# Performance work log

Measured on AMD Instinct MI355X. Metric: run time of the kernel, lower is better.

Reference implementation:

```python
import jax, jax.numpy as jnp
import numpy as np

D_MODEL = 768
N_HEADS_CFG = 12
D_STATE = 32
D_CONV = 4
EXPAND = 2
HEADDIM = D_MODEL // N_HEADS_CFG          # 64
D_INNER = EXPAND * D_MODEL                # 1536
NHEADS = D_INNER // HEADDIM               # 24 (Mamba2 internal heads)
CONV_DIM = D_INNER + 2 * D_STATE          # 1600
D_IN_PROJ = 2 * D_INNER + 2 * D_STATE + NHEADS  # 3160
EPS = 1e-5
B_SZ, SEQ = 2, 512


def rmsnorm(x, w):
    return x * jax.lax.rsqrt(jnp.mean(x * x, axis=-1, keepdims=True) + EPS) * w


def mamba2(u, Wi, cw, cb, dtb, Alog, Dp, nw, Wo):
    """Mamba2 mixer: in_proj -> causal depthwise conv(silu) -> selective scan -> gated RMSNorm -> out_proj."""
    b, l, _ = u.shape
    zxbcdt = u @ Wi.T                                   # [b,l,d_in_proj]
    z, xBC, dt = jnp.split(zxbcdt, [D_INNER, D_INNER + CONV_DIM], axis=-1)
    # causal depthwise conv over time
    xBC = jnp.transpose(xBC, (0, 2, 1))                 # [b,c,l]
    xBC = jax.lax.conv_general_dilated(
        xBC, cw[:, None, :], window_strides=(1,),
        padding=[(D_CONV - 1, 0)], feature_group_count=CONV_DIM)
    xBC = jax.nn.silu(jnp.transpose(xBC + cb[None, :, None], (0, 2, 1)))
    x, Bm, Cm = jnp.split(xBC, [D_INNER, D_INNER + D_STATE], axis=-1)
    x = x.reshape(b, l, NHEADS, HEADDIM)                # [b,l,h,p]
    dt = jax.nn.softplus(dt + dtb)                      # [b,l,h]
    A = -jnp.exp(Alog)                                  # [h]
    a = jnp.exp(dt * A)                                 # decay [b,l,h]
    # dt * x outer B  -> [b,l,h,p,n]
    dBx = (dt[..., None, None] * x[..., None]) * Bm[:, :, None, None, :]

    def combine(e1, e2):
        a1, h1 = e1
        a2, h2 = e2
        return (a1 * a2, a2[..., None, None] * h1 + h2)

    _, h = jax.lax.associative_scan(combine, (a, dBx), axis=1)  # h: [b,l,h,p,n]
    y = jnp.einsum('blhpn,bln->blhp', h, Cm) + Dp[None, None, :, None] * x
    y = y.reshape(b, l, D_INNER)
    y = rmsnorm(y * jax.nn.silu(z), nw)                 # gated RMSNorm
    return y @ Wo.T                                     # [b,l,d_model]


def _mamba_params(key, scale=0.02):
    ks = jax.random.split(key, 6)
    return dict(
        in_w=jax.random.normal(ks[0], (D_IN_PROJ, D_MODEL), jnp.float32) * scale,
        conv_w=jax.random.normal(ks[1], (CONV_DIM, D_CONV), jnp.float32) * scale,
        conv_b=jnp.zeros((CONV_DIM,), jnp.float32),
        dt_bias=jax.random.uniform(ks[2], (NHEADS,), jnp.float32, -4.0, -1.0),
        A_log=jnp.log(jax.random.uniform(ks[3], (NHEADS,), jnp.float32, 1.0, 16.0)),
        D=jnp.ones((NHEADS,), jnp.float32),
        norm_w=jnp.ones((D_INNER,), jnp.float32),
        out_w=jax.random.normal(ks[4], (D_MODEL, D_INNER), jnp.float32) * scale,
    )


def setup_inputs() -> dict:
    key = jax.random.key(0)
    kx, kf, kb, ko = jax.random.split(key, 4)
    f = _mamba_params(kf)
    bw = _mamba_params(kb)
    return {
        'x': jax.random.normal(kx, (B_SZ, SEQ, D_MODEL), jnp.float32),
        'norm_w': jnp.ones((D_MODEL,), jnp.float32),
        'fwd_in_w': f['in_w'], 'fwd_conv_w': f['conv_w'], 'fwd_conv_b': f['conv_b'],
        'fwd_dt_bias': f['dt_bias'], 'fwd_A_log': f['A_log'], 'fwd_D': f['D'],
        'fwd_norm_w': f['norm_w'], 'fwd_out_w': f['out_w'],
        'bwd_in_w': bw['in_w'], 'bwd_conv_w': bw['conv_w'], 'bwd_conv_b': bw['conv_b'],
        'bwd_dt_bias': bw['dt_bias'], 'bwd_A_log': bw['A_log'], 'bwd_D': bw['D'],
        'bwd_norm_w': bw['norm_w'], 'bwd_out_w': bw['out_w'],
        'out_proj_w': jax.random.normal(ko, (D_MODEL, 2 * D_MODEL), jnp.float32) * 0.02,
    }


def reference(x, norm_w,
              fwd_in_w, fwd_conv_w, fwd_conv_b, fwd_dt_bias, fwd_A_log, fwd_D, fwd_norm_w, fwd_out_w,
              bwd_in_w, bwd_conv_w, bwd_conv_b, bwd_dt_bias, bwd_A_log, bwd_D, bwd_norm_w, bwd_out_w,
              out_proj_w):
    h = rmsnorm(x, norm_w)
    f_out = mamba2(h, fwd_in_w, fwd_conv_w, fwd_conv_b, fwd_dt_bias, fwd_A_log, fwd_D, fwd_norm_w, fwd_out_w)
    b_out = mamba2(h[:, ::-1], bwd_in_w, bwd_conv_w, bwd_conv_b, bwd_dt_bias, bwd_A_log, bwd_D, bwd_norm_w, bwd_out_w)[:, ::-1]
    return x + jnp.concatenate([f_out, b_out], axis=-1) @ out_proj_w.T
```

## Files before the change

kernel.cpp:

```cpp
#include <hip/hip_runtime.h>
#include <hip/hip_bf16.h>

#define DMODEL 768
#define DINNER 1536
#define DSTATE 32
#define NHEADS 24
#define HEADDIM 64
#define CONVDIM 1600
#define DINPROJ 3160
#define NPAD 3200
#define SEQ 512
#define MROWS 1024
#define CL 64
#define NCH 8

typedef __attribute__((ext_vector_type(8))) short bf16x8;
typedef __attribute__((ext_vector_type(4))) float f32x4;

__device__ __forceinline__ ushort f2bs(float v) {
  __hip_bfloat16 b = __float2bfloat16(v);
  return __builtin_bit_cast(unsigned short, b);
}

__device__ __forceinline__ void gld16(const void* g, const void* l) {
  __builtin_amdgcn_global_load_lds((const __attribute__((address_space(1))) void*)g,
                                   (__attribute__((address_space(3))) void*)l, 16, 0, 0);
}

__device__ __forceinline__ float block_reduce_sum(float v, float* ws4) {
#pragma unroll
  for (int o = 32; o > 0; o >>= 1) v += __shfl_xor(v, o, 64);
  int wid = threadIdx.x >> 6;
  if ((threadIdx.x & 63) == 0) ws4[wid] = v;
  __syncthreads();
  return ws4[0] + ws4[1] + ws4[2] + ws4[3];
}

__global__ __launch_bounds__(256) void f2b_all(
    const float* __restrict__ s0, const float* __restrict__ s1,
    const float* __restrict__ s2, const float* __restrict__ s3,
    const float* __restrict__ s4, ushort* __restrict__ d) {
  constexpr size_t NP_IN = (size_t)NPAD * DMODEL;
  constexpr size_t NE_IN = (size_t)DINPROJ * DMODEL;
  constexpr size_t NE_O = (size_t)DMODEL * DINNER;
  size_t i = ((size_t)blockIdx.x * 256 + threadIdx.x) * 4;
  const float* src;
  size_t off, ne;
  if (i < NP_IN) { src = s0; off = i; ne = NE_IN; }
  else if (i < 2 * NP_IN) { src = s1; off = i - NP_IN; ne = NE_IN; }
  else if (i < 2 * NP_IN + NE_O) { src = s2; off = i - 2 * NP_IN; ne = NE_O; }
  else if (i < 2 * NP_IN + 2 * NE_O) { src = s3; off = i - 2 * NP_IN - NE_O; ne = NE_O; }
  else if (i < 2 * NP_IN + 3 * NE_O) { src = s4; off = i - 2 * NP_IN - 2 * NE_O; ne = NE_O; }
  else return;
  ushort* dp = d + i;
  if (off + 3 < ne) {
    float4 v = *(const float4*)(src + off);
    dp[0] = f2bs(v.x); dp[1] = f2bs(v.y); dp[2] = f2bs(v.z); dp[3] = f2bs(v.w);
  } else {
#pragma unroll
    for (int j = 0; j < 4; ++j) dp[j] = (off + j < ne) ? f2bs(src[off + j]) : (ushort)0;
  }
}

__global__ __launch_bounds__(256) void rmsnorm_in_kernel(
    const float* __restrict__ x, const float* __restrict__ w, ushort* __restrict__ h) {
  __shared__ float ws4[4];
  int m = blockIdx.x;
  const float* xr = x + (size_t)m * DMODEL;
  float v[3];
  float ss = 0.f;
#pragma unroll
  for (int i = 0; i < 3; ++i) {
    v[i] = xr[threadIdx.x + i * 256];
    ss += v[i] * v[i];
  }
  ss = block_reduce_sum(ss, ws4);
  float sc = rsqrtf(ss / (float)DMODEL + 1e-5f);
  ushort* hr = h + (size_t)m * DMODEL;
#pragma unroll
  for (int i = 0; i < 3; ++i) {
    int c = threadIdx.x + i * 256;
    hr[c] = f2bs(v[i] * sc * w[c]);
  }
}

template <int BM, int BN, bool ADD_X, bool OUT_BF16>
__global__ __launch_bounds__(256) void gemm2(
    const ushort* __restrict__ A, int lda, size_t aZ,
    const ushort* __restrict__ Bw, int ldb, size_t bZ,
    void* __restrict__ Cout, int ldc, size_t cZ,
    const float* __restrict__ X, int ldx, int K) {
  constexpr int AG = BM / 16;
  constexpr int BG = BN / 16;
  constexpr int MR = BM / 32;
  constexpr int NR = BN / 32;
  __shared__ ushort As[2][BM * 32];
  __shared__ ushort Bs[2][BN * 32];
  const int t = threadIdx.x, w = t >> 6, l = t & 63;
  const int m0 = blockIdx.y * BM, n0 = blockIdx.x * BN;
  const int wr = w >> 1, wc = w & 1;
  const int fr = l & 15, fq = l >> 4;
  const int sr = l >> 2, sc2 = (l & 3) * 8;
  const ushort* Ap = A + (size_t)blockIdx.z * aZ;
  const ushort* Bp = Bw + (size_t)blockIdx.z * bZ;

  auto stage = [&](int bb, int k0) {
#pragma unroll
    for (int g = w; g < AG + BG; g += 4) {
      if (g < AG) {
        int row = g * 16 + sr;
        gld16(Ap + (size_t)(m0 + row) * lda + k0 + sc2, (const char*)&As[bb][0] + g * 1024);
      } else {
        int gg = g - AG;
        int row = gg * 16 + sr;
        gld16(Bp + (size_t)(n0 + row) * ldb + k0 + sc2, (const char*)&Bs[bb][0] + gg * 1024);
      }
    }
  };

  f32x4 acc[MR][NR];
#pragma unroll
  for (int m = 0; m < MR; ++m)
#pragma unroll
    for (int n = 0; n < NR; ++n) acc[m][n] = (f32x4){0.f, 0.f, 0.f, 0.f};

  stage(0, 0);
  __syncthreads();
  int cur = 0;
  const int nk = K / 32;
  for (int k = 0; k < nk; ++k) {
    if (k + 1 < nk) stage(cur ^ 1, (k + 1) * 32);
    bf16x8 af[MR], bfr[NR];
#pragma unroll
    for (int m = 0; m < MR; ++m)
      af[m] = *(const bf16x8*)&As[cur][(wr * (BM / 2) + m * 16 + fr) * 32 + fq * 8];
#pragma unroll
    for (int n = 0; n < NR; ++n)
      bfr[n] = *(const bf16x8*)&Bs[cur][(wc * (BN / 2) + n * 16 + fr) * 32 + fq * 8];
#pragma unroll
    for (int m = 0; m < MR; ++m)
#pragma unroll
      for (int n = 0; n < NR; ++n)
        acc[m][n] = __builtin_amdgcn_mfma_f32_16x16x32_bf16(af[m], bfr[n], acc[m][n], 0, 0, 0);
    __syncthreads();
    cur ^= 1;
  }

#pragma unroll
  for (int m = 0; m < MR; ++m) {
#pragma unroll
    for (int n = 0; n < NR; ++n) {
      int col = n0 + wc * (BN / 2) + n * 16 + fr;
#pragma unroll
      for (int j = 0; j < 4; ++j) {
        int row = m0 + wr * (BM / 2) + m * 16 + fq * 4 + j;
        float v = acc[m][n][j];
        if (ADD_X) v += X[(size_t)row * ldx + col];
        if (OUT_BF16)
          ((ushort*)Cout + (size_t)blockIdx.z * cZ)[(size_t)row * ldc + col] = f2bs(v);
        else
          ((float*)Cout + (size_t)blockIdx.z * cZ)[(size_t)row * ldc + col] = v;
      }
    }
  }
}

__global__ __launch_bounds__(256) void conv_dt_kernel(
    const float* __restrict__ zx,
    const float* __restrict__ cw0, const float* __restrict__ cb0,
    const float* __restrict__ dtb0, const float* __restrict__ Al0,
    const float* __restrict__ cw1, const float* __restrict__ cb1,
    const float* __restrict__ dtb1, const float* __restrict__ Al1,
    float* __restrict__ xbc, float* __restrict__ dta) {
  int m = blockIdx.x;
  int dir = blockIdx.y;
  int l = m & (SEQ - 1);
  const float* cw = dir ? cw1 : cw0;
  const float* cb = dir ? cb1 : cb0;
  const float* zrow = zx + (size_t)m * 6400 + dir * 3200 + DINNER;
  float* xo = xbc + ((size_t)dir * MROWS + m) * CONVDIM;
  for (int c = threadIdx.x; c < CONVDIM; c += 256) {
    float acc = cb[c];
    if (dir == 0) {
#pragma unroll
      for (int d = 0; d < 4; ++d) {
        if (l - d >= 0) acc = fmaf(zrow[-(size_t)d * 6400 + c], cw[c * 4 + 3 - d], acc);
      }
    } else {
#pragma unroll
      for (int d = 0; d < 4; ++d) {
        if (l + d < SEQ) acc = fmaf(zrow[(size_t)d * 6400 + c], cw[c * 4 + 3 - d], acc);
      }
    }
    xo[c] = acc / (1.f + expf(-acc));
  }
  if (threadIdx.x < NHEADS) {
    int hh = threadIdx.x;
    const float* dtb = dir ? dtb1 : dtb0;
    const float* Al = dir ? Al1 : Al0;
    float v = zx[(size_t)m * 6400 + dir * 3200 + DINNER + CONVDIM + hh] + dtb[hh];
    float dt = (v > 20.f) ? v : log1pf(expf(v));
    float A = -expf(Al[hh]);
    dta[((size_t)dir * MROWS + m) * 48 + hh] = dt;
    dta[((size_t)dir * MROWS + m) * 48 + NHEADS + hh] = expf(dt * A);
  }
}

__global__ __launch_bounds__(256) void scan_phase1(
    const float* __restrict__ xbc, const float* __restrict__ dta,
    float* __restrict__ sbuf, float* __restrict__ abuf) {
  __shared__ float xs[CL][64];
  __shared__ float bcs[CL][64];
  __shared__ float das[CL][2];
  int c = blockIdx.x, bh = blockIdx.y, dir = blockIdx.z;
  int b = bh / NHEADS, h = bh % NHEADS;
  int t = threadIdx.x, p = t >> 2, q = t & 3;
  const float* xb = xbc + ((size_t)dir * MROWS + b * SEQ) * CONVDIM;
  int lrow = t >> 4, lcol = (t & 15) * 4;
#pragma unroll
  for (int r = 0; r < 4; ++r) {
    int s = r * 16 + lrow;
    int tau = c * CL + s;
    int prow = dir ? (SEQ - 1 - tau) : tau;
    const float* rowp = xb + (size_t)prow * CONVDIM;
    *(float4*)&xs[s][lcol] = *(const float4*)(rowp + h * HEADDIM + lcol);
    *(float4*)&bcs[s][lcol] = *(const float4*)(rowp + DINNER + lcol);
  }
  if (t < 128) {
    int s = t >> 1, wsel = t & 1;
    int tau = c * CL + s;
    int prow = dir ? (SEQ - 1 - tau) : tau;
    das[s][wsel] = dta[((size_t)dir * MROWS + b * SEQ + prow) * 48 + wsel * NHEADS + h];
  }
  __syncthreads();
  float hst[8];
#pragma unroll
  for (int j = 0; j < 8; ++j) hst[j] = 0.f;
  float alpha = 1.f;
#pragma unroll 8
  for (int s = 0; s < CL; ++s) {
    float xp = xs[s][p];
    float dt_s = das[s][0], a_s = das[s][1];
    float cx = dt_s * xp;
    alpha *= a_s;
    float4 B0 = *(const float4*)&bcs[s][q * 8];
    float4 B1 = *(const float4*)&bcs[s][q * 8 + 4];
    float Bv[8] = {B0.x, B0.y, B0.z, B0.w, B1.x, B1.y, B1.z, B1.w};
#pragma unroll
    for (int j = 0; j < 8; ++j) hst[j] = fmaf(a_s, hst[j], cx * Bv[j]);
  }
  float* sp = sbuf + (((size_t)(dir * 48 + bh)) * NCH + c) * 2048 + p * 32 + q * 8;
#pragma unroll
  for (int j = 0; j < 8; ++j) sp[j] = hst[j];
  if (t == 0) abuf[(dir * 48 + bh) * NCH + c] = alpha;
}

__global__ __launch_bounds__(256) void scan_phase2(float* __restrict__ sbuf,
                                                   const float* __restrict__ abuf) {
  int g = blockIdx.x;
  int t = threadIdx.x;
  float run[8];
#pragma unroll
  for (int j = 0; j < 8; ++j) run[j] = 0.f;
  size_t base = (size_t)g * NCH * 2048 + t * 8;
  for (int c = 0; c < NCH; ++c) {
    float* sp = sbuf + base + (size_t)c * 2048;
    float4 s0 = *(const float4*)sp;
    float4 s1 = *(const float4*)(sp + 4);
    float al = abuf[g * NCH + c];
    float4 r0 = {run[0], run[1], run[2], run[3]};
    float4 r1 = {run[4], run[5], run[6], run[7]};
    *(float4*)sp = r0;
    *(float4*)(sp + 4) = r1;
    float sv[8] = {s0.x, s0.y, s0.z, s0.w, s1.x, s1.y, s1.z, s1.w};
#pragma unroll
    for (int j = 0; j < 8; ++j) run[j] = fmaf(al, run[j], sv[j]);
  }
}

__global__ __launch_bounds__(256) void scan_phase3(
    const float* __restrict__ xbc, const float* __restrict__ dta,
    const float* __restrict__ sbuf,
    const float* __restrict__ Dp0, const float* __restrict__ Dp1,
    float* __restrict__ y) {
  __shared__ float xs[CL][64];
  __shared__ float bcs[CL][64];
  __shared__ float das[CL][2];
  int c = blockIdx.x, bh = blockIdx.y, dir = blockIdx.z;
  int b = bh / NHEADS, h = bh % NHEADS;
  int t = threadIdx.x, p = t >> 2, q = t & 3;
  const float* xb = xbc + ((size_t)dir * MROWS + b * SEQ) * CONVDIM;
  int lrow = t >> 4, lcol = (t & 15) * 4;
#pragma unroll
  for (int r = 0; r < 4; ++r) {
    int s = r * 16 + lrow;
    int tau = c * CL + s;
    int prow = dir ? (SEQ - 1 - tau) : tau;
    const float* rowp = xb + (size_t)prow * CONVDIM;
    *(float4*)&xs[s][lcol] = *(const float4*)(rowp + h * HEADDIM + lcol);
    *(float4*)&bcs[s][lcol] = *(const float4*)(rowp + DINNER + lcol);
  }
  if (t < 128) {
    int s = t >> 1, wsel = t & 1;
    int tau = c * CL + s;
    int prow = dir ? (SEQ - 1 - tau) : tau;
    das[s][wsel] = dta[((size_t)dir * MROWS + b * SEQ + prow) * 48 + wsel * NHEADS + h];
  }
  float hst[8];
  {
    const float* sp = sbuf + (((size_t)(dir * 48 + bh)) * NCH + c) * 2048 + p * 32 + q * 8;
    float4 h0 = *(const float4*)sp;
    float4 h1 = *(const float4*)(sp + 4);
    hst[0] = h0.x; hst[1] = h0.y; hst[2] = h0.z; hst[3] = h0.w;
    hst[4] = h1.x; hst[5] = h1.y; hst[6] = h1.z; hst[7] = h1.w;
  }
  float Dv = (dir ? Dp1 : Dp0)[h];
  __syncthreads();
#pragma unroll 8
  for (int s = 0; s < CL; ++s) {
    float xp = xs[s][p];
    float dt_s = das[s][0], a_s = das[s][1];
    float cx = dt_s * xp;
    float4 B0 = *(const float4*)&bcs[s][q * 8];
    float4 B1 = *(const float4*)&bcs[s][q * 8 + 4];
    float4 C0 = *(const float4*)&bcs[s][32 + q * 8];
    float4 C1 = *(const float4*)&bcs[s][32 + q * 8 + 4];
    float Bv[8] = {B0.x, B0.y, B0.z, B0.w, B1.x, B1.y, B1.z, B1.w};
    float Cv[8] = {C0.x, C0.y, C0.z, C0.w, C1.x, C1.y, C1.z, C1.w};
    float acc = 0.f;
#pragma unroll
    for (int j = 0; j < 8; ++j) {
      hst[j] = fmaf(a_s, hst[j], cx * Bv[j]);
      acc = fmaf(hst[j], Cv[j], acc);
    }
    acc += __shfl_xor(acc, 1, 64);
    acc += __shfl_xor(acc, 2, 64);
    if (q == 0) {
      int tau = c * CL + s;
      int prow = dir ? (SEQ - 1 - tau) : tau;
      y[((size_t)dir * MROWS + b * SEQ + prow) * DINNER + h * HEADDIM + p] = fmaf(Dv, xp, acc);
    }
  }
}

__global__ __launch_bounds__(256) void gated_norm_kernel(
    const float* __restrict__ y,
    const float* __restrict__ zx,
    const float* __restrict__ nw0, const float* __restrict__ nw1,
    ushort* __restrict__ yn) {
  __shared__ float ws4[4];
  int m = blockIdx.x;
  int dir = blockIdx.y;
  const float* nw = dir ? nw1 : nw0;
  float g[6];
  float ss = 0.f;
#pragma unroll
  for (int i = 0; i < 6; ++i) {
    int c = threadIdx.x + i * 256;
    float yv = y[((size_t)dir * MROWS + m) * DINNER + c];
    float zv = zx[(size_t)m * 6400 + dir * 3200 + c];
    float gg = yv * (zv / (1.f + expf(-zv)));
    g[i] = gg;
    ss += gg * gg;
  }
  ss = block_reduce_sum(ss, ws4);
  float sc = rsqrtf(ss / (float)DINNER + 1e-5f);
#pragma unroll
  for (int i = 0; i < 6; ++i) {
    int c = threadIdx.x + i * 256;
    yn[((size_t)dir * MROWS + m) * DINNER + c] = f2bs(g[i] * sc * nw[c]);
  }
}

extern "C" void kernel_launch(void* const* d_in, const int* in_sizes, int n_in,
                              void* d_out, int out_size, void* d_ws, size_t ws_size,
                              hipStream_t stream) {
  const float* x = (const float*)d_in[0];
  const float* norm_w = (const float*)d_in[1];
  const float* in_w[2] = {(const float*)d_in[2], (const float*)d_in[10]};
  const float* conv_w[2] = {(const float*)d_in[3], (const float*)d_in[11]};
  const float* conv_b[2] = {(const float*)d_in[4], (const float*)d_in[12]};
  const float* dt_bias[2] = {(const float*)d_in[5], (const float*)d_in[13]};
  const float* A_log[2] = {(const float*)d_in[6], (const float*)d_in[14]};
  const float* Dp[2] = {(const float*)d_in[7], (const float*)d_in[15]};
  const float* nw[2] = {(const float*)d_in[8], (const float*)d_in[16]};
  const float* out_w[2] = {(const float*)d_in[9], (const float*)d_in[17]};
  const float* proj_w = (const float*)d_in[18];
  float* out = (float*)d_out;

  char* p = (char*)d_ws;
  float* zx = (float*)p;    p += (size_t)MROWS * 6400 * 4;
  float* xbc = (float*)p;   p += (size_t)2 * MROWS * CONVDIM * 4;
  float* dta = (float*)p;   p += (size_t)2 * MROWS * 48 * 4;
  float* y = (float*)p;     p += (size_t)2 * MROWS * DINNER * 4;
  float* sbuf = (float*)p;  p += (size_t)96 * NCH * 2048 * 4;
  float* abuf = (float*)p;  p += (size_t)96 * NCH * 4;
  ushort* h = (ushort*)p;   p += (size_t)MROWS * DMODEL * 2;
  ushort* yn = (ushort*)p;  p += (size_t)2 * MROWS * DINNER * 2;
  ushort* cat = (ushort*)p; p += (size_t)MROWS * DINNER * 2;
  ushort* wi = (ushort*)p;  p += (size_t)2 * NPAD * DMODEL * 2;
  ushort* wo = (ushort*)p;  p += (size_t)2 * DMODEL * DINNER * 2;
  ushort* wp = (ushort*)p;  p += (size_t)DMODEL * DINNER * 2;

  {
    size_t tot = 2 * (size_t)NPAD * DMODEL + 3 * (size_t)DMODEL * DINNER;
    f2b_all<<<(tot / 4 + 255) / 256, 256, 0, stream>>>(in_w[0], in_w[1], out_w[0], out_w[1],
                                                       proj_w, wi);
  }

  rmsnorm_in_kernel<<<MROWS, 256, 0, stream>>>(x, norm_w, h);

  {
    dim3 g(6400 / 128, MROWS / 128, 1);
    gemm2<128, 128, false, false><<<g, 256, 0, stream>>>(h, DMODEL, 0, wi, DMODEL, 0,
                                                         zx, 6400, 0, nullptr, 0, DMODEL);
  }

  conv_dt_kernel<<<dim3(MROWS, 2), 256, 0, stream>>>(
      zx, conv_w[0], conv_b[0], dt_bias[0], A_log[0],
      conv_w[1], conv_b[1], dt_bias[1], A_log[1], xbc, dta);

  scan_phase1<<<dim3(NCH, 48, 2), 256, 0, stream>>>(xbc, dta, sbuf, abuf);
  scan_phase2<<<96, 256, 0, stream>>>(sbuf, abuf);
  scan_phase3<<<dim3(NCH, 48, 2), 256, 0, stream>>>(xbc, dta, sbuf, Dp[0], Dp[1], y);

  gated_norm_kernel<<<dim3(MROWS, 2), 256, 0, stream>>>(y, zx, nw[0], nw[1], yn);

  {
    dim3 g(DMODEL / 64, MROWS / 128, 2);
    gemm2<128, 64, false, true><<<g, 256, 0, stream>>>(
        yn, DINNER, (size_t)MROWS * DINNER, wo, DINNER, (size_t)DMODEL * DINNER,
        cat, DINNER, (size_t)DMODEL, nullptr, 0, DINNER);
  }

  {
    dim3 g(DMODEL / 64, MROWS / 64, 1);
    gemm2<64, 64, true, false><<<g, 256, 0, stream>>>(cat, DINNER, 0, wp, DINNER, 0,
                                                      out, DMODEL, 0, x, DMODEL, DINNER);
  }
}
```

Before: 132.5 us.

## Fuse fp32-to-bf16 weight conversion into GEMM loads and merge scan phases

Drops the standalone weight conversion kernel. The GEMMs now read fp32 weights directly, converting them to bf16 in registers before writing them to LDS, with the next B tile loaded into registers while the current MFMAs run. Removes the scan_phase2 launch: each phase-3 block rebuilds its starting state by serially combining the earlier chunk states. This saves two launches and the round trip of the converted weights, but the GEMMs now read twice the B bytes per tile and do conversion work themselves. Later chunks also repeat the prefix work.

```diff
diff --git a/kernel.cpp b/kernel.cpp
--- a/kernel.cpp
+++ b/kernel.cpp
@@ -8,7 +8,6 @@
 #define HEADDIM 64
 #define CONVDIM 1600
 #define DINPROJ 3160
-#define NPAD 3200
 #define SEQ 512
 #define MROWS 1024
 #define CL 64
@@ -34,32 +33,6 @@
   if ((threadIdx.x & 63) == 0) ws4[wid] = v;
   __syncthreads();
   return ws4[0] + ws4[1] + ws4[2] + ws4[3];
-}
-
-__global__ __launch_bounds__(256) void f2b_all(
-    const float* __restrict__ s0, const float* __restrict__ s1,
-    const float* __restrict__ s2, const float* __restrict__ s3,
-    const float* __restrict__ s4, ushort* __restrict__ d) {
-  constexpr size_t NP_IN = (size_t)NPAD * DMODEL;
-  constexpr size_t NE_IN = (size_t)DINPROJ * DMODEL;
-  constexpr size_t NE_O = (size_t)DMODEL * DINNER;
-  size_t i = ((size_t)blockIdx.x * 256 + threadIdx.x) * 4;
-  const float* src;
-  size_t off, ne;
-  if (i < NP_IN) { src = s0; off = i; ne = NE_IN; }
-  else if (i < 2 * NP_IN) { src = s1; off = i - NP_IN; ne = NE_IN; }
-  else if (i < 2 * NP_IN + NE_O) { src = s2; off = i - 2 * NP_IN; ne = NE_O; }
-  else if (i < 2 * NP_IN + 2 * NE_O) { src = s3; off = i - 2 * NP_IN - NE_O; ne = NE_O; }
-  else if (i < 2 * NP_IN + 3 * NE_O) { src = s4; off = i - 2 * NP_IN - 2 * NE_O; ne = NE_O; }
-  else return;
-  ushort* dp = d + i;
-  if (off + 3 < ne) {
-    float4 v = *(const float4*)(src + off);
-    dp[0] = f2bs(v.x); dp[1] = f2bs(v.y); dp[2] = f2bs(v.z); dp[3] = f2bs(v.w);
-  } else {
-#pragma unroll
-    for (int j = 0; j < 4; ++j) dp[j] = (off + j < ne) ? f2bs(src[off + j]) : (ushort)0;
-  }
 }
 
 __global__ __launch_bounds__(256) void rmsnorm_in_kernel(
@@ -84,14 +57,15 @@
   }
 }
 
-template <int BM, int BN, bool ADD_X, bool OUT_BF16>
-__global__ __launch_bounds__(256) void gemm2(
+template <int BM, int BN, int BSEL, bool ADD_X, bool OUT_BF16>
+__global__ __launch_bounds__(256) void gemm3(
     const ushort* __restrict__ A, int lda, size_t aZ,
-    const ushort* __restrict__ Bw, int ldb, size_t bZ,
+    const float* __restrict__ B0, const float* __restrict__ B1, int ldb,
     void* __restrict__ Cout, int ldc, size_t cZ,
     const float* __restrict__ X, int ldx, int K) {
   constexpr int AG = BM / 16;
   constexpr int BG = BN / 16;
+  constexpr int BPW = BG / 4;
   constexpr int MR = BM / 32;
   constexpr int NR = BN / 32;
   __shared__ ushort As[2][BM * 32];
@@ -102,34 +76,61 @@
   const int fr = l & 15, fq = l >> 4;
   const int sr = l >> 2, sc2 = (l & 3) * 8;
   const ushort* Ap = A + (size_t)blockIdx.z * aZ;
-  const ushort* Bp = Bw + (size_t)blockIdx.z * bZ;
-
-  auto stage = [&](int bb, int k0) {
-#pragma unroll
-    for (int g = w; g < AG + BG; g += 4) {
-      if (g < AG) {
-        int row = g * 16 + sr;
-        gld16(Ap + (size_t)(m0 + row) * lda + k0 + sc2, (const char*)&As[bb][0] + g * 1024);
-      } else {
-        int gg = g - AG;
-        int row = gg * 16 + sr;
-        gld16(Bp + (size_t)(n0 + row) * ldb + k0 + sc2, (const char*)&Bs[bb][0] + gg * 1024);
-      }
-    }
+
+  auto brow = [&](int r) -> const float* {
+    if (BSEL == 0) return B0 + (size_t)r * ldb;
+    if (BSEL == 1) {
+      int rr = (r < 3200) ? r : r - 3200;
+      if (rr >= DINPROJ) rr = DINPROJ - 1;
+      return ((r < 3200) ? B0 : B1) + (size_t)rr * ldb;
+    }
+    return (blockIdx.z ? B1 : B0) + (size_t)r * ldb;
   };
 
+  float4 bv[BPW][2];
+  auto bload = [&](int k0) {
+#pragma unroll
+    for (int i = 0; i < BPW; ++i) {
+      int g = w + i * 4;
+      const float* rp = brow(n0 + g * 16 + sr) + k0 + sc2;
+      bv[i][0] = *(const float4*)rp;
+      bv[i][1] = *(const float4*)(rp + 4);
+    }
+  };
+  auto bwrite = [&](int bb) {
+#pragma unroll
+    for (int i = 0; i < BPW; ++i) {
+      int g = w + i * 4;
+      uint u0 = (uint)f2bs(bv[i][0].x) | ((uint)f2bs(bv[i][0].y) << 16);
+      uint u1 = (uint)f2bs(bv[i][0].z) | ((uint)f2bs(bv[i][0].w) << 16);
+      uint u2 = (uint)f2bs(bv[i][1].x) | ((uint)f2bs(bv[i][1].y) << 16);
+      uint u3 = (uint)f2bs(bv[i][1].z) | ((uint)f2bs(bv[i][1].w) << 16);
+      *(uint4*)&Bs[bb][g * 512 + l * 8] = (uint4){u0, u1, u2, u3};
+    }
+  };
+  auto astage = [&](int bb, int k0) {
+#pragma unroll
+    for (int g = w; g < AG; g += 4)
+      gld16(Ap + (size_t)(m0 + g * 16 + sr) * lda + k0 + sc2, (const char*)&As[bb][0] + g * 1024);
+  };
+
   f32x4 acc[MR][NR];
 #pragma unroll
   for (int m = 0; m < MR; ++m)
 #pragma unroll
     for (int n = 0; n < NR; ++n) acc[m][n] = (f32x4){0.f, 0.f, 0.f, 0.f};
 
-  stage(0, 0);
+  bload(0);
+  astage(0, 0);
+  bwrite(0);
   __syncthreads();
   int cur = 0;
   const int nk = K / 32;
   for (int k = 0; k < nk; ++k) {
-    if (k + 1 < nk) stage(cur ^ 1, (k + 1) * 32);
+    if (k + 1 < nk) {
+      bload((k + 1) * 32);
+      astage(cur ^ 1, (k + 1) * 32);
+    }
     bf16x8 af[MR], bfr[NR];
 #pragma unroll
     for (int m = 0; m < MR; ++m)
@@ -142,6 +143,7 @@
 #pragma unroll
       for (int n = 0; n < NR; ++n)
         acc[m][n] = __builtin_amdgcn_mfma_f32_16x16x32_bf16(af[m], bfr[n], acc[m][n], 0, 0, 0);
+    if (k + 1 < nk) bwrite(cur ^ 1);
     __syncthreads();
     cur ^= 1;
   }
@@ -250,37 +252,14 @@
     for (int j = 0; j < 8; ++j) hst[j] = fmaf(a_s, hst[j], cx * Bv[j]);
   }
   float* sp = sbuf + (((size_t)(dir * 48 + bh)) * NCH + c) * 2048 + p * 32 + q * 8;
-#pragma unroll
-  for (int j = 0; j < 8; ++j) sp[j] = hst[j];
+  *(float4*)sp = (float4){hst[0], hst[1], hst[2], hst[3]};
+  *(float4*)(sp + 4) = (float4){hst[4], hst[5], hst[6], hst[7]};
   if (t == 0) abuf[(dir * 48 + bh) * NCH + c] = alpha;
 }
 
-__global__ __launch_bounds__(256) void scan_phase2(float* __restrict__ sbuf,
-                                                   const float* __restrict__ abuf) {
-  int g = blockIdx.x;
-  int t = threadIdx.x;
-  float run[8];
-#pragma unroll
-  for (int j = 0; j < 8; ++j) run[j] = 0.f;
-  size_t base = (size_t)g * NCH * 2048 + t * 8;
-  for (int c = 0; c < NCH; ++c) {
-    float* sp = sbuf + base + (size_t)c * 2048;
-    float4 s0 = *(const float4*)sp;
-    float4 s1 = *(const float4*)(sp + 4);
-    float al = abuf[g * NCH + c];
-    float4 r0 = {run[0], run[1], run[2], run[3]};
-    float4 r1 = {run[4], run[5], run[6], run[7]};
-    *(float4*)sp = r0;
-    *(float4*)(sp + 4) = r1;
-    float sv[8] = {s0.x, s0.y, s0.z, s0.w, s1.x, s1.y, s1.z, s1.w};
-#pragma unroll
-    for (int j = 0; j < 8; ++j) run[j] = fmaf(al, run[j], sv[j]);
-  }
-}
-
-__global__ __launch_bounds__(256) void scan_phase3(
+__global__ __launch_bounds__(256) void scan_phase3b(
     const float* __restrict__ xbc, const float* __restrict__ dta,
-    const float* __restrict__ sbuf,
+    const float* __restrict__ sbuf, const float* __restrict__ abuf,
     const float* __restrict__ Dp0, const float* __restrict__ Dp1,
     float* __restrict__ y) {
   __shared__ float xs[CL][64];
@@ -306,14 +285,20 @@
     int prow = dir ? (SEQ - 1 - tau) : tau;
     das[s][wsel] = dta[((size_t)dir * MROWS + b * SEQ + prow) * 48 + wsel * NHEADS + h];
   }
+
   float hst[8];
-  {
-    const float* sp = sbuf + (((size_t)(dir * 48 + bh)) * NCH + c) * 2048 + p * 32 + q * 8;
-    float4 h0 = *(const float4*)sp;
-    float4 h1 = *(const float4*)(sp + 4);
-    hst[0] = h0.x; hst[1] = h0.y; hst[2] = h0.z; hst[3] = h0.w;
-    hst[4] = h1.x; hst[5] = h1.y; hst[6] = h1.z; hst[7] = h1.w;
-  }
+#pragma unroll
+  for (int j = 0; j < 8; ++j) hst[j] = 0.f;
+  for (int cc = 0; cc < c; ++cc) {
+    const float* sp = sbuf + (((size_t)(dir * 48 + bh)) * NCH + cc) * 2048 + p * 32 + q * 8;
+    float4 s0 = *(const float4*)sp;
+    float4 s1 = *(const float4*)(sp + 4);
+    float al = abuf[(dir * 48 + bh) * NCH + cc];
+    float sv[8] = {s0.x, s0.y, s0.z, s0.w, s1.x, s1.y, s1.z, s1.w};
+#pragma unroll
+    for (int j = 0; j < 8; ++j) hst[j] = fmaf(al, hst[j], sv[j]);
+  }
+
   float Dv = (dir ? Dp1 : Dp0)[h];
   __syncthreads();
 #pragma unroll 8
@@ -398,22 +383,13 @@
   ushort* h = (ushort*)p;   p += (size_t)MROWS * DMODEL * 2;
   ushort* yn = (ushort*)p;  p += (size_t)2 * MROWS * DINNER * 2;
   ushort* cat = (ushort*)p; p += (size_t)MROWS * DINNER * 2;
-  ushort* wi = (ushort*)p;  p += (size_t)2 * NPAD * DMODEL * 2;
-  ushort* wo = (ushort*)p;  p += (size_t)2 * DMODEL * DINNER * 2;
-  ushort* wp = (ushort*)p;  p += (size_t)DMODEL * DINNER * 2;
-
-  {
-    size_t tot = 2 * (size_t)NPAD * DMODEL + 3 * (size_t)DMODEL * DINNER;
-    f2b_all<<<(tot / 4 + 255) / 256, 256, 0, stream>>>(in_w[0], in_w[1], out_w[0], out_w[1],
-                                                       proj_w, wi);
-  }
 
   rmsnorm_in_kernel<<<MROWS, 256, 0, stream>>>(x, norm_w, h);
 
   {
     dim3 g(6400 / 128, MROWS / 128, 1);
-    gemm2<128, 128, false, false><<<g, 256, 0, stream>>>(h, DMODEL, 0, wi, DMODEL, 0,
-                                                         zx, 6400, 0, nullptr, 0, DMODEL);
+    gemm3<128, 128, 1, false, false><<<g, 256, 0, stream>>>(
+        h, DMODEL, 0, in_w[0], in_w[1], DMODEL, zx, 6400, 0, nullptr, 0, DMODEL);
   }
 
   conv_dt_kernel<<<dim3(MROWS, 2), 256, 0, stream>>>(
@@ -421,21 +397,20 @@
       conv_w[1], conv_b[1], dt_bias[1], A_log[1], xbc, dta);
 
   scan_phase1<<<dim3(NCH, 48, 2), 256, 0, stream>>>(xbc, dta, sbuf, abuf);
-  scan_phase2<<<96, 256, 0, stream>>>(sbuf, abuf);
-  scan_phase3<<<dim3(NCH, 48, 2), 256, 0, stream>>>(xbc, dta, sbuf, Dp[0], Dp[1], y);
+  scan_phase3b<<<dim3(NCH, 48, 2), 256, 0, stream>>>(xbc, dta, sbuf, abuf, Dp[0], Dp[1], y);
 
   gated_norm_kernel<<<dim3(MROWS, 2), 256, 0, stream>>>(y, zx, nw[0], nw[1], yn);
 
   {
     dim3 g(DMODEL / 64, MROWS / 128, 2);
-    gemm2<128, 64, false, true><<<g, 256, 0, stream>>>(
-        yn, DINNER, (size_t)MROWS * DINNER, wo, DINNER, (size_t)DMODEL * DINNER,
+    gemm3<128, 64, 2, false, true><<<g, 256, 0, stream>>>(
+        yn, DINNER, (size_t)MROWS * DINNER, out_w[0], out_w[1], DINNER,
         cat, DINNER, (size_t)DMODEL, nullptr, 0, DINNER);
   }
 
   {
     dim3 g(DMODEL / 64, MROWS / 64, 1);
-    gemm2<64, 64, true, false><<<g, 256, 0, stream>>>(cat, DINNER, 0, wp, DINNER, 0,
-                                                      out, DMODEL, 0, x, DMODEL, DINNER);
-  }
-}
+    gemm3<64, 64, 0, true, false><<<g, 256, 0, stream>>>(
+        cat, DINNER, 0, proj_w, nullptr, DINNER, out, DMODEL, 0, x, DMODEL, DINNER);
+  }
+}
```

New measurement: 143.7 us. +8.5%, slower.
